# Kernel optimization log

Measured on AMD Instinct MI355X. Metric: run time of the kernel, lower is better.

Reference implementation:

```python
import jax, jax.numpy as jnp
import numpy as np

SQRT_N = 64  # sqrt_n; padded sequence length n = SQRT_N**2 = 4096


def _perm(x, r):
    # rearrange '... (m n) -> ... (n m)' with m = n = r
    return x.reshape(*x.shape[:-1], r, r).swapaxes(-1, -2).reshape(x.shape)


def _blockdiag_matmul(x, w):
    # torch.einsum('bnm,...bm->...bn', w, x.view(..., b, m)).reshape(x.shape)
    b, _, m = w.shape
    xv = x.reshape(*x.shape[:-1], b, m)
    return jnp.einsum('bnm,...bm->...bn', w, xv).reshape(x.shape)


def _monarch(x, L, R, r):
    x = _perm(x, r)
    x = _blockdiag_matmul(x, L)
    x = _perm(x, r)
    x = _blockdiag_matmul(x, R)
    return _perm(x, r)


def setup_inputs() -> dict:
    key = jax.random.key(0)
    ks = jax.random.split(key, 9)
    B, S, H, D = 8, 4096, 8, 64
    r = SQRT_N
    bound_b = 1.0 / r
    # kaiming_uniform_(a=sqrt(5)) on a (r, r, r) tensor: fan_in = r*r,
    # gain = sqrt(2/(1+5)) = sqrt(1/3), bound = gain*sqrt(3/fan_in) = 1/r
    bound_w = 1.0 / r
    return {
        'queries': jax.random.normal(ks[0], (B, S, H, D), jnp.float32),
        'keys': jax.random.normal(ks[1], (B, S, H, D), jnp.float32),
        'values': jax.random.normal(ks[2], (B, S, H, D), jnp.float32),
        'M1L': jax.random.uniform(ks[3], (r, r, r), jnp.float32, -bound_w, bound_w),
        'M1R': jax.random.uniform(ks[4], (r, r, r), jnp.float32, -bound_w, bound_w),
        'M2L': jax.random.uniform(ks[5], (r, r, r), jnp.float32, -bound_w, bound_w),
        'M2R': jax.random.uniform(ks[6], (r, r, r), jnp.float32, -bound_w, bound_w),
        'b1': jax.random.uniform(ks[7], (r * r,), jnp.float32, -bound_b, bound_b),
        'b2': jax.random.uniform(ks[8], (r * r,), jnp.float32, -bound_b, bound_b),
    }


def reference(queries, keys, values, M1L, M1R, M2L, M2R, b1, b2):
    r = SQRT_N
    B, S, H, D = queries.shape
    n2 = r * r
    pad = n2 - S
    # (B,S,H,D) -> (B,H,D,S)
    q = jnp.transpose(queries, (0, 2, 3, 1))
    k = jnp.transpose(keys, (0, 2, 3, 1))
    v = jnp.transpose(values, (0, 2, 3, 1))
    cfg = [(0, 0)] * 3 + [(0, pad)]
    q = jnp.pad(q, cfg)
    k = jnp.pad(k, cfg)
    # A = M1(q) * k + b1 ; dropout is identity (eval / p=0)
    A = _monarch(q, M1L, M1R, r) * k + b1
    A = _monarch(A, M2L, M2R, r) + b2
    Y = A[..., :S] * v  # (B,H,D,S)
    return Y
```

## Files before the change

kernel.cpp:

```cpp
#include <hip/hip_runtime.h>
#include <cstdint>
#include <cstddef>

typedef unsigned short u16;
typedef __attribute__((ext_vector_type(8))) short bf16x8;
typedef __attribute__((ext_vector_type(4))) float f32x4;

#define S_LEN 4096

__device__ __forceinline__ float bf2f(u16 u) {
  return __uint_as_float(((unsigned)u) << 16);
}
__device__ __forceinline__ u16 f2bf(float f) {
  unsigned x = __float_as_uint(f);
  return (u16)((x + 0x7fffu + ((x >> 16) & 1u)) >> 16);
}

__device__ __forceinline__ int ltelem(int c, int r) {
  int swz = ((r >> 3) ^ (c & 7) ^ ((c >> 3) & 7)) & 7;
  return (c << 6) | (swz << 3) | (r & 7);
}

__device__ __forceinline__ bf16x8 load_afrag(const float* __restrict__ Wrow, int ks, int lane) {
  const float4* p = (const float4*)(Wrow + ks * 32 + ((lane >> 4) << 3));
  float4 a = p[0], b = p[1];
  bf16x8 r;
  r[0] = (short)f2bf(a.x); r[1] = (short)f2bf(a.y);
  r[2] = (short)f2bf(a.z); r[3] = (short)f2bf(a.w);
  r[4] = (short)f2bf(b.x); r[5] = (short)f2bf(b.y);
  r[6] = (short)f2bf(b.z); r[7] = (short)f2bf(b.w);
  return r;
}

__device__ __forceinline__ bf16x8 load_bfrag(const ushort* LT, int fc, int ks, int lane) {
  int c = (fc << 4) + (lane & 15);
  int kg = (ks << 2) + (lane >> 4);
  int base = (c << 6) | (((kg ^ (c & 7) ^ ((c >> 3) & 7)) & 7) << 3);
  return *(const bf16x8*)&LT[base];
}

__device__ __forceinline__ void mm16x64(const float* __restrict__ Arow, const ushort* LT,
                                        int lane, f32x4 acc[4]) {
#pragma unroll
  for (int ks = 0; ks < 2; ++ks) {
    bf16x8 af = load_afrag(Arow, ks, lane);
#pragma unroll
    for (int fc = 0; fc < 4; ++fc) {
      bf16x8 bf = load_bfrag(LT, fc, ks, lane);
      acc[fc] = __builtin_amdgcn_mfma_f32_16x16x32_bf16(af, bf, acc[fc], 0, 0, 0);
    }
  }
}

__global__ __launch_bounds__(256) void k_m1(const float* __restrict__ q,
                                            const float* __restrict__ L1,
                                            u16* __restrict__ T1) {
  const int B = blockIdx.x, bh = blockIdx.y;
  const int b = bh >> 3, h = bh & 7;
  __shared__ ushort LT[4096];
  const int tid = threadIdx.x, w = tid >> 6, lane = tid & 63;
  {
    const int m = tid >> 2, ch = tid & 3;
    const float* qrow = q + ((((size_t)b * S_LEN + (size_t)m * 64 + B) * 8 + h) << 6);
#pragma unroll
    for (int i = 0; i < 4; ++i) {
      float4 v = *(const float4*)(qrow + ch * 16 + i * 4);
      int c0 = ch * 16 + i * 4;
      LT[ltelem(c0 + 0, m)] = f2bf(v.x);
      LT[ltelem(c0 + 1, m)] = f2bf(v.y);
      LT[ltelem(c0 + 2, m)] = f2bf(v.z);
      LT[ltelem(c0 + 3, m)] = f2bf(v.w);
    }
  }
  __syncthreads();
  f32x4 acc[4] = {};
  mm16x64(L1 + (((size_t)B << 6) + (w << 4) + (lane & 15)) * 64, LT, lane, acc);
#pragma unroll
  for (int fc = 0; fc < 4; ++fc) {
    int d = (fc << 4) + (lane & 15);
#pragma unroll
    for (int r = 0; r < 4; ++r) {
      int n = (w << 4) + ((lane >> 4) << 2) + r;
      T1[(((size_t)bh * 64 + n) * 64 + B) * 64 + d] = f2bf(acc[fc][r]);
    }
  }
}

__global__ __launch_bounds__(256) void k_m2b(const u16* __restrict__ T1,
                                             const float* __restrict__ R1,
                                             const float* __restrict__ L2,
                                             const float* __restrict__ keys,
                                             const float* __restrict__ b1,
                                             u16* __restrict__ T2) {
  const int n = blockIdx.x, bh = blockIdx.y;
  const int b = bh >> 3, h = bh & 7;
  __shared__ ushort LT[4096];
  __shared__ ushort LT2[4096];
  __shared__ ushort KT[4096];
  const int tid = threadIdx.x, w = tid >> 6, lane = tid & 63;
  {
    const int rowi = tid >> 2, ch = tid & 3;
    const u16* src = T1 + (((size_t)bh * 64 + n) * 64 + rowi) * 64 + ch * 16;
    u16 buf[16];
    *(uint4*)&buf[0] = *(const uint4*)(src);
    *(uint4*)&buf[8] = *(const uint4*)(src + 8);
#pragma unroll
    for (int e = 0; e < 16; ++e) LT[ltelem(ch * 16 + e, rowi)] = buf[e];
  }
#pragma unroll
  for (int i = 0; i < 4; ++i) {
    int idx = i * 256 + tid;
    int p = idx >> 4, c4 = (idx & 15) * 4;
    float4 kv = *(const float4*)&keys[(((size_t)b * S_LEN + p * 64 + n) * 8 + h) * 64 + c4];
    KT[ltelem(c4 + 0, p)] = f2bf(kv.x);
    KT[ltelem(c4 + 1, p)] = f2bf(kv.y);
    KT[ltelem(c4 + 2, p)] = f2bf(kv.z);
    KT[ltelem(c4 + 3, p)] = f2bf(kv.w);
  }
  __syncthreads();
  f32x4 acc[4] = {};
  mm16x64(R1 + ((size_t)n * 64 + (w << 4) + (lane & 15)) * 64, LT, lane, acc);
  float b1v[4];
#pragma unroll
  for (int r = 0; r < 4; ++r)
    b1v[r] = b1[((w << 4) + ((lane >> 4) << 2) + r) * 64 + n];
#pragma unroll
  for (int fc = 0; fc < 4; ++fc) {
    int d = (fc << 4) + (lane & 15);
#pragma unroll
    for (int r = 0; r < 4; ++r) {
      int p = (w << 4) + ((lane >> 4) << 2) + r;
      float kvv = bf2f(KT[ltelem(d, p)]);
      LT2[ltelem(d, p)] = f2bf(acc[fc][r] * kvv + b1v[r]);
    }
  }
  __syncthreads();
  f32x4 acc2[4] = {};
  mm16x64(L2 + ((size_t)n * 64 + (w << 4) + (lane & 15)) * 64, LT2, lane, acc2);
#pragma unroll
  for (int fc = 0; fc < 4; ++fc) {
    int d = (fc << 4) + (lane & 15);
#pragma unroll
    for (int r = 0; r < 4; ++r) {
      int n2 = (w << 4) + ((lane >> 4) << 2) + r;
      T2[(((size_t)bh * 64 + n2) * 64 + n) * 64 + d] = f2bf(acc2[fc][r]);
    }
  }
}

__global__ __launch_bounds__(256) void k_m3b(const u16* __restrict__ T2,
                                             const float* __restrict__ R2,
                                             const float* __restrict__ vals,
                                             const float* __restrict__ b2,
                                             u16* __restrict__ Yp) {
  const int np = blockIdx.x, bh = blockIdx.y;
  const int b = bh >> 3, h = bh & 7;
  __shared__ ushort LT[4096];
  __shared__ ushort VT[4096];
  const int tid = threadIdx.x, w = tid >> 6, lane = tid & 63;
  {
    const int rowi = tid >> 2, ch = tid & 3;
    const u16* src = T2 + (((size_t)bh * 64 + np) * 64 + rowi) * 64 + ch * 16;
    u16 buf[16];
    *(uint4*)&buf[0] = *(const uint4*)(src);
    *(uint4*)&buf[8] = *(const uint4*)(src + 8);
#pragma unroll
    for (int e = 0; e < 16; ++e) LT[ltelem(ch * 16 + e, rowi)] = buf[e];
  }
#pragma unroll
  for (int i = 0; i < 4; ++i) {
    int idx = i * 256 + tid;
    int p = idx >> 4, c4 = (idx & 15) * 4;
    float4 vv = *(const float4*)&vals[(((size_t)b * S_LEN + p * 64 + np) * 8 + h) * 64 + c4];
    VT[ltelem(c4 + 0, p)] = f2bf(vv.x);
    VT[ltelem(c4 + 1, p)] = f2bf(vv.y);
    VT[ltelem(c4 + 2, p)] = f2bf(vv.z);
    VT[ltelem(c4 + 3, p)] = f2bf(vv.w);
  }
  __syncthreads();
  f32x4 acc[4] = {};
  mm16x64(R2 + ((size_t)np * 64 + (w << 4) + (lane & 15)) * 64, LT, lane, acc);
  float b2v[4];
#pragma unroll
  for (int r = 0; r < 4; ++r)
    b2v[r] = b2[((w << 4) + ((lane >> 4) << 2) + r) * 64 + np];
#pragma unroll
  for (int fc = 0; fc < 4; ++fc) {
    int d = (fc << 4) + (lane & 15);
#pragma unroll
    for (int r = 0; r < 4; ++r) {
      int p = (w << 4) + ((lane >> 4) << 2) + r;
      float vv = bf2f(VT[ltelem(d, p)]);
      Yp[(((size_t)bh * 64 + np) * 64 + p) * 64 + d] = f2bf((acc[fc][r] + b2v[r]) * vv);
    }
  }
}

__global__ __launch_bounds__(256) void k_tr(const u16* __restrict__ Yp,
                                            float* __restrict__ out) {
  const int p = blockIdx.x, bh = blockIdx.y;
  __shared__ ushort YT[4096];
  const int tid = threadIdx.x;
#pragma unroll
  for (int i = 0; i < 2; ++i) {
    int idx = i * 256 + tid;
    int np = idx >> 3, q8 = idx & 7;
    uint4 vv = *(const uint4*)&Yp[(((size_t)bh * 64 + np) * 64 + p) * 64 + q8 * 8];
    *(uint4*)&YT[ltelem(np, q8 * 8)] = vv;
  }
  __syncthreads();
#pragma unroll
  for (int i = 0; i < 4; ++i) {
    int idx = i * 256 + tid;
    int d = idx >> 4, np0 = (idx & 15) * 4;
    float4 o;
    o.x = bf2f(YT[ltelem(np0 + 0, d)]);
    o.y = bf2f(YT[ltelem(np0 + 1, d)]);
    o.z = bf2f(YT[ltelem(np0 + 2, d)]);
    o.w = bf2f(YT[ltelem(np0 + 3, d)]);
    *(float4*)&out[((size_t)bh * 64 + d) * S_LEN + p * 64 + np0] = o;
  }
}

extern "C" void kernel_launch(void* const* d_in, const int* in_sizes, int n_in,
                              void* d_out, int out_size, void* d_ws, size_t ws_size,
                              hipStream_t stream) {
  const float* q   = (const float*)d_in[0];
  const float* k   = (const float*)d_in[1];
  const float* v   = (const float*)d_in[2];
  const float* M1L = (const float*)d_in[3];
  const float* M1R = (const float*)d_in[4];
  const float* M2L = (const float*)d_in[5];
  const float* M2R = (const float*)d_in[6];
  const float* b1  = (const float*)d_in[7];
  const float* b2  = (const float*)d_in[8];

  u16* T1 = (u16*)d_ws;
  u16* T2 = T1 + (size_t)64 * 64 * 64 * 64;
  u16* Yp = T1;

  dim3 blk(256);
  dim3 grd(64, 64);
  k_m1 <<<grd, blk, 0, stream>>>(q, M1L, T1);
  k_m2b<<<grd, blk, 0, stream>>>(T1, M1R, M2L, k, b1, T2);
  k_m3b<<<grd, blk, 0, stream>>>(T2, M2R, v, b2, Yp);
  k_tr <<<grd, blk, 0, stream>>>(Yp, (float*)d_out);
}
```

Before: 116.1 us.

## Prepack Monarch weights into bf16 MFMA fragments and keep keys/values in registers

Adds a prep kernel that converts the four fp32 Monarch weight tensors into bf16, laid out in MFMA A-fragment order, stored in the output buffer as scratch. The matmul kernels then load each fragment with one 16-byte read instead of reading fp32 rows and converting them per block. The keys and values tiles are now read straight into registers in the accumulator layout, which removes the LDS staging buffers and the fp32-to-bf16 rounding of k and v. The trade-offs are an extra kernel launch and uncoalesced 4-byte global loads for k and v.

```diff
diff --git a/kernel.cpp b/kernel.cpp
--- a/kernel.cpp
+++ b/kernel.cpp
@@ -19,17 +19,6 @@
 __device__ __forceinline__ int ltelem(int c, int r) {
   int swz = ((r >> 3) ^ (c & 7) ^ ((c >> 3) & 7)) & 7;
   return (c << 6) | (swz << 3) | (r & 7);
-}
-
-__device__ __forceinline__ bf16x8 load_afrag(const float* __restrict__ Wrow, int ks, int lane) {
-  const float4* p = (const float4*)(Wrow + ks * 32 + ((lane >> 4) << 3));
-  float4 a = p[0], b = p[1];
-  bf16x8 r;
-  r[0] = (short)f2bf(a.x); r[1] = (short)f2bf(a.y);
-  r[2] = (short)f2bf(a.z); r[3] = (short)f2bf(a.w);
-  r[4] = (short)f2bf(b.x); r[5] = (short)f2bf(b.y);
-  r[6] = (short)f2bf(b.z); r[7] = (short)f2bf(b.w);
-  return r;
 }
 
 __device__ __forceinline__ bf16x8 load_bfrag(const ushort* LT, int fc, int ks, int lane) {
@@ -39,11 +28,16 @@
   return *(const bf16x8*)&LT[base];
 }
 
-__device__ __forceinline__ void mm16x64(const float* __restrict__ Arow, const ushort* LT,
-                                        int lane, f32x4 acc[4]) {
+__device__ __forceinline__ bf16x8 apk_frag(const u16* __restrict__ APK, int mat, int gr,
+                                           int ks, int lane) {
+  return *(const bf16x8*)&APK[(((((mat << 8) + gr) << 1) + ks) << 9) + lane * 8];
+}
+
+__device__ __forceinline__ void mm16x64(const u16* __restrict__ APK, int mat, int gr,
+                                        const ushort* LT, int lane, f32x4 acc[4]) {
 #pragma unroll
   for (int ks = 0; ks < 2; ++ks) {
-    bf16x8 af = load_afrag(Arow, ks, lane);
+    bf16x8 af = apk_frag(APK, mat, gr, ks, lane);
 #pragma unroll
     for (int fc = 0; fc < 4; ++fc) {
       bf16x8 bf = load_bfrag(LT, fc, ks, lane);
@@ -52,8 +46,25 @@
   }
 }
 
+__global__ __launch_bounds__(256) void k_prep(const float* __restrict__ W0,
+                                              const float* __restrict__ W1,
+                                              const float* __restrict__ W2,
+                                              const float* __restrict__ W3,
+                                              u16* __restrict__ APK) {
+  const int gr = blockIdx.x, mat = blockIdx.y;
+  const float* W = (mat == 0) ? W0 : (mat == 1) ? W1 : (mat == 2) ? W2 : W3;
+  const int t = threadIdx.x;
+  const int lane = t & 63, ks = (t >> 6) & 1, half = t >> 7;
+  const int row = gr * 16 + (lane & 15);
+  const int k0 = ks * 32 + ((lane >> 4) << 3) + half * 4;
+  float4 v = *(const float4*)&W[row * 64 + k0];
+  ushort4 o;
+  o.x = f2bf(v.x); o.y = f2bf(v.y); o.z = f2bf(v.z); o.w = f2bf(v.w);
+  *(ushort4*)&APK[((((((mat << 8) + gr) << 1) + ks) << 6) + lane) * 8 + half * 4] = o;
+}
+
 __global__ __launch_bounds__(256) void k_m1(const float* __restrict__ q,
-                                            const float* __restrict__ L1,
+                                            const u16* __restrict__ APK,
                                             u16* __restrict__ T1) {
   const int B = blockIdx.x, bh = blockIdx.y;
   const int b = bh >> 3, h = bh & 7;
@@ -74,7 +85,7 @@
   }
   __syncthreads();
   f32x4 acc[4] = {};
-  mm16x64(L1 + (((size_t)B << 6) + (w << 4) + (lane & 15)) * 64, LT, lane, acc);
+  mm16x64(APK, 0, B * 4 + w, LT, lane, acc);
 #pragma unroll
   for (int fc = 0; fc < 4; ++fc) {
     int d = (fc << 4) + (lane & 15);
@@ -87,8 +98,7 @@
 }
 
 __global__ __launch_bounds__(256) void k_m2b(const u16* __restrict__ T1,
-                                             const float* __restrict__ R1,
-                                             const float* __restrict__ L2,
+                                             const u16* __restrict__ APK,
                                              const float* __restrict__ keys,
                                              const float* __restrict__ b1,
                                              u16* __restrict__ T2) {
@@ -96,8 +106,18 @@
   const int b = bh >> 3, h = bh & 7;
   __shared__ ushort LT[4096];
   __shared__ ushort LT2[4096];
-  __shared__ ushort KT[4096];
   const int tid = threadIdx.x, w = tid >> 6, lane = tid & 63;
+
+  float kreg[4][4], b1v[4];
+#pragma unroll
+  for (int r = 0; r < 4; ++r) {
+    int p = (w << 4) + ((lane >> 4) << 2) + r;
+    b1v[r] = b1[p * 64 + n];
+    const float* krow = &keys[(((size_t)b * S_LEN + p * 64 + n) * 8 + h) << 6];
+#pragma unroll
+    for (int fc = 0; fc < 4; ++fc)
+      kreg[fc][r] = krow[(fc << 4) + (lane & 15)];
+  }
   {
     const int rowi = tid >> 2, ch = tid & 3;
     const u16* src = T1 + (((size_t)bh * 64 + n) * 64 + rowi) * 64 + ch * 16;
@@ -107,36 +127,21 @@
 #pragma unroll
     for (int e = 0; e < 16; ++e) LT[ltelem(ch * 16 + e, rowi)] = buf[e];
   }
-#pragma unroll
-  for (int i = 0; i < 4; ++i) {
-    int idx = i * 256 + tid;
-    int p = idx >> 4, c4 = (idx & 15) * 4;
-    float4 kv = *(const float4*)&keys[(((size_t)b * S_LEN + p * 64 + n) * 8 + h) * 64 + c4];
-    KT[ltelem(c4 + 0, p)] = f2bf(kv.x);
-    KT[ltelem(c4 + 1, p)] = f2bf(kv.y);
-    KT[ltelem(c4 + 2, p)] = f2bf(kv.z);
-    KT[ltelem(c4 + 3, p)] = f2bf(kv.w);
-  }
   __syncthreads();
   f32x4 acc[4] = {};
-  mm16x64(R1 + ((size_t)n * 64 + (w << 4) + (lane & 15)) * 64, LT, lane, acc);
-  float b1v[4];
-#pragma unroll
-  for (int r = 0; r < 4; ++r)
-    b1v[r] = b1[((w << 4) + ((lane >> 4) << 2) + r) * 64 + n];
+  mm16x64(APK, 1, n * 4 + w, LT, lane, acc);
 #pragma unroll
   for (int fc = 0; fc < 4; ++fc) {
     int d = (fc << 4) + (lane & 15);
 #pragma unroll
     for (int r = 0; r < 4; ++r) {
       int p = (w << 4) + ((lane >> 4) << 2) + r;
-      float kvv = bf2f(KT[ltelem(d, p)]);
-      LT2[ltelem(d, p)] = f2bf(acc[fc][r] * kvv + b1v[r]);
+      LT2[ltelem(d, p)] = f2bf(acc[fc][r] * kreg[fc][r] + b1v[r]);
     }
   }
   __syncthreads();
   f32x4 acc2[4] = {};
-  mm16x64(L2 + ((size_t)n * 64 + (w << 4) + (lane & 15)) * 64, LT2, lane, acc2);
+  mm16x64(APK, 2, n * 4 + w, LT2, lane, acc2);
 #pragma unroll
   for (int fc = 0; fc < 4; ++fc) {
     int d = (fc << 4) + (lane & 15);
@@ -149,15 +154,25 @@
 }
 
 __global__ __launch_bounds__(256) void k_m3b(const u16* __restrict__ T2,
-                                             const float* __restrict__ R2,
+                                             const u16* __restrict__ APK,
                                              const float* __restrict__ vals,
                                              const float* __restrict__ b2,
                                              u16* __restrict__ Yp) {
   const int np = blockIdx.x, bh = blockIdx.y;
   const int b = bh >> 3, h = bh & 7;
   __shared__ ushort LT[4096];
-  __shared__ ushort VT[4096];
   const int tid = threadIdx.x, w = tid >> 6, lane = tid & 63;
+
+  float vreg[4][4], b2v[4];
+#pragma unroll
+  for (int r = 0; r < 4; ++r) {
+    int p = (w << 4) + ((lane >> 4) << 2) + r;
+    b2v[r] = b2[p * 64 + np];
+    const float* vrow = &vals[(((size_t)b * S_LEN + p * 64 + np) * 8 + h) << 6];
+#pragma unroll
+    for (int fc = 0; fc < 4; ++fc)
+      vreg[fc][r] = vrow[(fc << 4) + (lane & 15)];
+  }
   {
     const int rowi = tid >> 2, ch = tid & 3;
     const u16* src = T2 + (((size_t)bh * 64 + np) * 64 + rowi) * 64 + ch * 16;
@@ -167,31 +182,16 @@
 #pragma unroll
     for (int e = 0; e < 16; ++e) LT[ltelem(ch * 16 + e, rowi)] = buf[e];
   }
-#pragma unroll
-  for (int i = 0; i < 4; ++i) {
-    int idx = i * 256 + tid;
-    int p = idx >> 4, c4 = (idx & 15) * 4;
-    float4 vv = *(const float4*)&vals[(((size_t)b * S_LEN + p * 64 + np) * 8 + h) * 64 + c4];
-    VT[ltelem(c4 + 0, p)] = f2bf(vv.x);
-    VT[ltelem(c4 + 1, p)] = f2bf(vv.y);
-    VT[ltelem(c4 + 2, p)] = f2bf(vv.z);
-    VT[ltelem(c4 + 3, p)] = f2bf(vv.w);
-  }
   __syncthreads();
   f32x4 acc[4] = {};
-  mm16x64(R2 + ((size_t)np * 64 + (w << 4) + (lane & 15)) * 64, LT, lane, acc);
-  float b2v[4];
-#pragma unroll
-  for (int r = 0; r < 4; ++r)
-    b2v[r] = b2[((w << 4) + ((lane >> 4) << 2) + r) * 64 + np];
+  mm16x64(APK, 3, np * 4 + w, LT, lane, acc);
 #pragma unroll
   for (int fc = 0; fc < 4; ++fc) {
     int d = (fc << 4) + (lane & 15);
 #pragma unroll
     for (int r = 0; r < 4; ++r) {
       int p = (w << 4) + ((lane >> 4) << 2) + r;
-      float vv = bf2f(VT[ltelem(d, p)]);
-      Yp[(((size_t)bh * 64 + np) * 64 + p) * 64 + d] = f2bf((acc[fc][r] + b2v[r]) * vv);
+      Yp[(((size_t)bh * 64 + np) * 64 + p) * 64 + d] = f2bf((acc[fc][r] + b2v[r]) * vreg[fc][r]);
     }
   }
 }
@@ -238,11 +238,13 @@
   u16* T1 = (u16*)d_ws;
   u16* T2 = T1 + (size_t)64 * 64 * 64 * 64;
   u16* Yp = T1;
+  u16* APK = (u16*)d_out;
 
   dim3 blk(256);
   dim3 grd(64, 64);
-  k_m1 <<<grd, blk, 0, stream>>>(q, M1L, T1);
-  k_m2b<<<grd, blk, 0, stream>>>(T1, M1R, M2L, k, b1, T2);
-  k_m3b<<<grd, blk, 0, stream>>>(T2, M2R, v, b2, Yp);
+  k_prep<<<dim3(256, 4), blk, 0, stream>>>(M1L, M1R, M2L, M2R, APK);
+  k_m1 <<<grd, blk, 0, stream>>>(q, APK, T1);
+  k_m2b<<<grd, blk, 0, stream>>>(T1, APK, k, b1, T2);
+  k_m3b<<<grd, blk, 0, stream>>>(T2, APK, v, b2, Yp);
   k_tr <<<grd, blk, 0, stream>>>(Yp, (float*)d_out);
 }
```

New measurement: 109.4 us. -5.8%, faster.
